# Performance work log

Hardware: AMD Instinct MI355X
Metric: run time of the kernel (lower is better)

The kernel has to match this reference:

```python
import jax, jax.numpy as jnp
import numpy as np
import math

B, S, D, H = 2, 2048, 512, 8
HD = D // H

def setup_inputs() -> dict:
    key = jax.random.key(0)
    ks = jax.random.split(key, 13)
    scale = 1.0 / math.sqrt(D)
    inp = {
        "q_in": jax.random.normal(ks[0], (B, S, D), jnp.float32),
        "k_in": jax.random.normal(ks[1], (B, S, D), jnp.float32),
        "v_in": jax.random.normal(ks[2], (B, S, D), jnp.float32),
        "mask": jax.random.randint(ks[3], (B, 1, S, S), 0, 2, jnp.int32),
        "W1": jax.random.uniform(ks[4], (D, D), jnp.float32, -scale, scale),
        "b1": jax.random.uniform(ks[5], (D,), jnp.float32, -scale, scale),
        "W2": jax.random.uniform(ks[6], (D, D), jnp.float32, -scale, scale),
        "b2": jax.random.uniform(ks[7], (D,), jnp.float32, -scale, scale),
        "W3": jax.random.uniform(ks[8], (D, D), jnp.float32, -scale, scale),
        "b3": jax.random.uniform(ks[9], (D,), jnp.float32, -scale, scale),
        "Wo": jax.random.uniform(ks[10], (D, D), jnp.float32, -scale, scale),
        "bo": jax.random.uniform(ks[11], (D,), jnp.float32, -scale, scale),
    }
    return inp

def reference(q_in, k_in, v_in, mask, W1, b1, W2, b2, W3, b3, Wo, bo):
    # Linear projections (torch Linear: y = x @ W.T + b)
    q = q_in @ W1.T + b1  # [B,S,D]
    k = k_in @ W2.T + b2
    v = v_in @ W3.T + b3
    # split heads -> [B,H,S,HD]
    def split(x):
        return x.reshape(B, S, H, HD).transpose(0, 2, 1, 3)
    q, k, v = split(q), split(k), split(v)
    scores = jnp.einsum("bhqd,bhkd->bhqk", q, k) / math.sqrt(HD)
    scores = jnp.where(mask == 0, jnp.float32(-1e9), scores)
    attn = jax.nn.softmax(scores, axis=-1)
    out = jnp.einsum("bhqk,bhkd->bhqd", attn, v)  # [B,H,S,HD]
    out = out.transpose(0, 2, 1, 3).reshape(B, S, D)
    return out @ Wo.T + bo
```

## Files before the change

kernel.cpp:

```cpp
#include <hip/hip_runtime.h>
#include <hip/hip_bf16.h>
#include <math.h>

constexpr int B_ = 2, S_ = 2048, D_ = 512, H_ = 8, HD_ = 64;
constexpr int M_ = B_ * S_;
constexpr int NT_ = S_ / 64;
constexpr int NSPLIT = 2;
constexpr int NT2 = NT_ / NSPLIT;
constexpr int ROWS = B_ * S_ * H_;

typedef short s16x8 __attribute__((ext_vector_type(8)));
typedef float f32x4 __attribute__((ext_vector_type(4)));
typedef unsigned short u16;
typedef unsigned long long u64;

#define SWZ(b) ((b) ^ ((((b) >> 7) & 7) << 4))

constexpr float SCL = 0.18033688f;
constexpr float FIXM = 12.0f;

static __device__ __forceinline__ unsigned int cvt_pk2(float lo, float hi) {
  __hip_bfloat162 h = __float22bfloat162_rn(make_float2(lo, hi));
  return *(unsigned int*)&h;
}
static __device__ __forceinline__ u16 cvt1(float f) {
  __hip_bfloat16 h = __float2bfloat16(f);
  return *(u16*)&h;
}
static __device__ __forceinline__ uint4 pack8(float4 a, float4 b) {
  uint4 r;
  r.x = cvt_pk2(a.x, a.y); r.y = cvt_pk2(a.z, a.w);
  r.z = cvt_pk2(b.x, b.y); r.w = cvt_pk2(b.z, b.w);
  return r;
}

#define QKV_STEP(BUF, T)                                                      \
  {                                                                           \
    const bool more_ = ((T) < 7);                                             \
    if (more_) {                                                              \
      const int o4 = ((T) + 1) * 16;                                          \
      fx[0] = Xb[o4]; fx[1] = Xb[o4 + 1]; fx[2] = Xb[o4 + 2]; fx[3] = Xb[o4 + 3]; \
      fw[0] = Wb[o4]; fw[1] = Wb[o4 + 1]; fw[2] = Wb[o4 + 2]; fw[3] = Wb[o4 + 3]; \
    }                                                                         \
    __builtin_amdgcn_s_setprio(1);                                            \
    _Pragma("unroll")                                                         \
    for (int kw = 0; kw < 2; ++kw) {                                          \
      s16x8 af0 = *(const s16x8*)(shb + SWZ((BUF)*16384 + (wm*32 + l15)*128 + kw*64 + lg*16)); \
      s16x8 af1 = *(const s16x8*)(shb + SWZ((BUF)*16384 + (wm*32 + 16 + l15)*128 + kw*64 + lg*16)); \
      s16x8 bf0 = *(const s16x8*)(shb + SWZ((BUF)*16384 + 8192 + (wn*32 + l15)*128 + kw*64 + lg*16)); \
      s16x8 bf1 = *(const s16x8*)(shb + SWZ((BUF)*16384 + 8192 + (wn*32 + 16 + l15)*128 + kw*64 + lg*16)); \
      acc[0][0] = __builtin_amdgcn_mfma_f32_16x16x32_bf16(af0, bf0, acc[0][0], 0, 0, 0); \
      acc[0][1] = __builtin_amdgcn_mfma_f32_16x16x32_bf16(af0, bf1, acc[0][1], 0, 0, 0); \
      acc[1][0] = __builtin_amdgcn_mfma_f32_16x16x32_bf16(af1, bf0, acc[1][0], 0, 0, 0); \
      acc[1][1] = __builtin_amdgcn_mfma_f32_16x16x32_bf16(af1, bf1, acc[1][1], 0, 0, 0); \
    }                                                                         \
    __builtin_amdgcn_s_setprio(0);                                            \
    if (more_) {                                                              \
      char* p_ = shb + ((BUF) ^ 1) * 16384;                                   \
      *(uint4*)(p_ + SWZ(awb)) = pack8(fx[0], fx[1]);                         \
      *(uint4*)(p_ + SWZ(awb + 16)) = pack8(fx[2], fx[3]);                    \
      *(uint4*)(p_ + SWZ(bwb)) = pack8(fw[0], fw[1]);                         \
      *(uint4*)(p_ + SWZ(bwb + 16)) = pack8(fw[2], fw[3]);                    \
    }                                                                         \
    __syncthreads();                                                          \
  }

__global__ __launch_bounds__(256) void gemm_qkv(
    const float* __restrict__ Xq, const float* __restrict__ Wq,
    const float* __restrict__ bq, u16* __restrict__ Yq,
    const float* __restrict__ Xk, const float* __restrict__ Wk,
    const float* __restrict__ bk, u16* __restrict__ Yk,
    const float* __restrict__ Xv, const float* __restrict__ Wv,
    const float* __restrict__ bv, u16* __restrict__ Yv,
    const int* __restrict__ mask, u64* __restrict__ mbits)
{
  const float* X; const float* W; const float* bias; u16* Y;
  const int z = blockIdx.z;
  if (z == 0)      { X = Xq; W = Wq; bias = bq; Y = Yq; }
  else if (z == 1) { X = Xk; W = Wk; bias = bk; Y = Yk; }
  else             { X = Xv; W = Wv; bias = bv; Y = Yv; }

  __shared__ __align__(128) u16 SH[2][2][64][64];
  char* shb = (char*)SH;

  const int tid = threadIdx.x;
  const int lane = tid & 63, w = tid >> 6;
  const int l15 = lane & 15, lg = lane >> 4;
  const int wm = w >> 1, wn = w & 1;
  const int m0 = blockIdx.x * 64, n0 = blockIdx.y * 64;
  const int sr = tid >> 2, sc = (tid & 3) * 16;

  const float4* Xb = (const float4*)&X[(size_t)(m0 + sr) * D_ + sc];
  const float4* Wb = (const float4*)&W[(size_t)(n0 + sr) * D_ + sc];
  const int awb = sr * 128 + (tid & 3) * 32;
  const int bwb = 8192 + sr * 128 + (tid & 3) * 32;

  f32x4 acc[2][2];
#pragma unroll
  for (int i = 0; i < 2; ++i)
#pragma unroll
    for (int j = 0; j < 2; ++j) acc[i][j] = (f32x4){0.f, 0.f, 0.f, 0.f};

  float4 fx[4], fw[4];
#pragma unroll
  for (int i = 0; i < 4; ++i) { fx[i] = Xb[i]; fw[i] = Wb[i]; }
  {
    char* p = shb;
    *(uint4*)(p + SWZ(awb)) = pack8(fx[0], fx[1]);
    *(uint4*)(p + SWZ(awb + 16)) = pack8(fx[2], fx[3]);
    *(uint4*)(p + SWZ(bwb)) = pack8(fw[0], fw[1]);
    *(uint4*)(p + SWZ(bwb + 16)) = pack8(fw[2], fw[3]);
  }
  __syncthreads();

#pragma unroll 1
  for (int tt = 0; tt < 8; tt += 2) {
    QKV_STEP(0, tt)
    QKV_STEP(1, tt + 1)
  }

  float bias_v[2];
  bias_v[0] = bias[n0 + wn * 32 + l15];
  bias_v[1] = bias[n0 + wn * 32 + 16 + l15];
  const float oscale = (z == 0) ? SCL : 1.0f;

  if (z != 2) {
#pragma unroll
    for (int am = 0; am < 2; ++am)
#pragma unroll
      for (int bn = 0; bn < 2; ++bn)
#pragma unroll
        for (int j = 0; j < 4; ++j) {
          const int row = m0 + wm * 32 + am * 16 + lg * 4 + j;
          const int col = n0 + wn * 32 + bn * 16 + l15;
          Y[(size_t)row * D_ + col] = cvt1((acc[am][bn][j] + bias_v[bn]) * oscale);
        }
  } else {
#pragma unroll
    for (int am = 0; am < 2; ++am)
#pragma unroll
      for (int bn = 0; bn < 2; ++bn) {
        const int dd = wn * 32 + bn * 16 + l15;
        const int sl = wm * 32 + am * 16 + lg * 4;
        ushort4 pk;
        pk.x = cvt1(acc[am][bn][0] + bias_v[bn]);
        pk.y = cvt1(acc[am][bn][1] + bias_v[bn]);
        pk.z = cvt1(acc[am][bn][2] + bias_v[bn]);
        pk.w = cvt1(acc[am][bn][3] + bias_v[bn]);
        *(ushort4*)(shb + SWZ(dd * 128 + sl * 2)) = pk;
      }
    __syncthreads();
    const int batch = m0 >> 11, sb = m0 & (S_ - 1);
    const int cr = sr * 128 + (tid & 3) * 32;
    uint4 c0 = *(uint4*)(shb + SWZ(cr));
    uint4 c1 = *(uint4*)(shb + SWZ(cr + 16));
    u16* dst = &Y[(((size_t)batch * H_ + blockIdx.y) * 64 + sr) * S_ + sb + sc];
    *(uint4*)dst = c0;
    *(uint4*)(dst + 8) = c1;
  }

  {
    const int bid = blockIdx.x + blockIdx.y * gridDim.x +
                    blockIdx.z * gridDim.x * gridDim.y;
    const int gw = bid * 4 + w;
    const int nslots = B_ * S_ * NT_;
#pragma unroll 1
    for (int s = gw * 4; s < nslots; s += 6144 * 4) {
      int v0 = mask[(size_t)(s + 0) * 64 + lane];
      int v1 = (s + 1 < nslots) ? mask[(size_t)(s + 1) * 64 + lane] : 0;
      int v2 = (s + 2 < nslots) ? mask[(size_t)(s + 2) * 64 + lane] : 0;
      int v3 = (s + 3 < nslots) ? mask[(size_t)(s + 3) * 64 + lane] : 0;
      u64 b0 = __ballot(v0 != 0);
      u64 b1 = __ballot(v1 != 0);
      u64 b2 = __ballot(v2 != 0);
      u64 b3 = __ballot(v3 != 0);
      if (lane == 0) {
        mbits[s] = b0;
        if (s + 1 < nslots) mbits[s + 1] = b1;
        if (s + 2 < nslots) mbits[s + 2] = b2;
        if (s + 3 < nslots) mbits[s + 3] = b3;
      }
    }
  }
}

#define OPROJ_STEP(BUF, T)                                                    \
  {                                                                           \
    const bool more_ = ((T) < 7);                                             \
    if (more_) {                                                              \
      const int k0 = ((T) + 1) * 64;                                          \
      ax[0] = ((const uint4*)(Xb + k0))[0];                                   \
      ax[1] = ((const uint4*)(Xb + k0))[1];                                   \
      const int o4 = ((T) + 1) * 16;                                          \
      fw[0] = Wb[o4]; fw[1] = Wb[o4 + 1]; fw[2] = Wb[o4 + 2]; fw[3] = Wb[o4 + 3]; \
    }                                                                         \
    __builtin_amdgcn_s_setprio(1);                                            \
    _Pragma("unroll")                                                         \
    for (int kw = 0; kw < 2; ++kw) {                                          \
      s16x8 af0 = *(const s16x8*)(shb + SWZ((BUF)*16384 + (wm*32 + l15)*128 + kw*64 + lg*16)); \
      s16x8 af1 = *(const s16x8*)(shb + SWZ((BUF)*16384 + (wm*32 + 16 + l15)*128 + kw*64 + lg*16)); \
      s16x8 bf0 = *(const s16x8*)(shb + SWZ((BUF)*16384 + 8192 + (wn*32 + l15)*128 + kw*64 + lg*16)); \
      s16x8 bf1 = *(const s16x8*)(shb + SWZ((BUF)*16384 + 8192 + (wn*32 + 16 + l15)*128 + kw*64 + lg*16)); \
      acc[0][0] = __builtin_amdgcn_mfma_f32_16x16x32_bf16(af0, bf0, acc[0][0], 0, 0, 0); \
      acc[0][1] = __builtin_amdgcn_mfma_f32_16x16x32_bf16(af0, bf1, acc[0][1], 0, 0, 0); \
      acc[1][0] = __builtin_amdgcn_mfma_f32_16x16x32_bf16(af1, bf0, acc[1][0], 0, 0, 0); \
      acc[1][1] = __builtin_amdgcn_mfma_f32_16x16x32_bf16(af1, bf1, acc[1][1], 0, 0, 0); \
    }                                                                         \
    __builtin_amdgcn_s_setprio(0);                                            \
    if (more_) {                                                              \
      char* p_ = shb + ((BUF) ^ 1) * 16384;                                   \
      *(uint4*)(p_ + SWZ(awb)) = ax[0];                                       \
      *(uint4*)(p_ + SWZ(awb + 16)) = ax[1];                                  \
      *(uint4*)(p_ + SWZ(bwb)) = pack8(fw[0], fw[1]);                         \
      *(uint4*)(p_ + SWZ(bwb + 16)) = pack8(fw[2], fw[3]);                    \
    }                                                                         \
    __syncthreads();                                                          \
  }

__global__ __launch_bounds__(256) void gemm_oproj(
    const u16* __restrict__ X, const float* __restrict__ W,
    const float* __restrict__ bias, float* __restrict__ Y)
{
  __shared__ __align__(128) u16 SH[2][2][64][64];
  char* shb = (char*)SH;

  const int tid = threadIdx.x;
  const int lane = tid & 63, w = tid >> 6;
  const int l15 = lane & 15, lg = lane >> 4;
  const int wm = w >> 1, wn = w & 1;
  const int m0 = blockIdx.x * 64, n0 = blockIdx.y * 64;
  const int sr = tid >> 2, sc = (tid & 3) * 16;

  const u16* Xb = X + (size_t)(m0 + sr) * D_ + sc;
  const float4* Wb = (const float4*)&W[(size_t)(n0 + sr) * D_ + sc];
  const int awb = sr * 128 + (tid & 3) * 32;
  const int bwb = 8192 + sr * 128 + (tid & 3) * 32;

  f32x4 acc[2][2];
#pragma unroll
  for (int i = 0; i < 2; ++i)
#pragma unroll
    for (int j = 0; j < 2; ++j) acc[i][j] = (f32x4){0.f, 0.f, 0.f, 0.f};

  uint4 ax[2]; float4 fw[4];
  ax[0] = ((const uint4*)Xb)[0]; ax[1] = ((const uint4*)Xb)[1];
#pragma unroll
  for (int i = 0; i < 4; ++i) fw[i] = Wb[i];
  {
    char* p = shb;
    *(uint4*)(p + SWZ(awb)) = ax[0];
    *(uint4*)(p + SWZ(awb + 16)) = ax[1];
    *(uint4*)(p + SWZ(bwb)) = pack8(fw[0], fw[1]);
    *(uint4*)(p + SWZ(bwb + 16)) = pack8(fw[2], fw[3]);
  }
  __syncthreads();

#pragma unroll 1
  for (int tt = 0; tt < 8; tt += 2) {
    OPROJ_STEP(0, tt)
    OPROJ_STEP(1, tt + 1)
  }

  float bias_v[2];
  bias_v[0] = bias[n0 + wn * 32 + l15];
  bias_v[1] = bias[n0 + wn * 32 + 16 + l15];
#pragma unroll
  for (int am = 0; am < 2; ++am)
#pragma unroll
    for (int bn = 0; bn < 2; ++bn)
#pragma unroll
      for (int j = 0; j < 4; ++j) {
        const int row = m0 + wm * 32 + am * 16 + lg * 4 + j;
        const int col = n0 + wn * 32 + bn * 16 + l15;
        Y[(size_t)row * D_ + col] = acc[am][bn][j] + bias_v[bn];
      }
}

__global__ __launch_bounds__(256) void attn_mfma(
    const u16* __restrict__ qp, const u16* __restrict__ kp,
    const u16* __restrict__ vt, const u64* __restrict__ mbits,
    float* __restrict__ po, float* __restrict__ pm, float* __restrict__ pl)
{
  const int b = blockIdx.z >> 1, half = blockIdx.z & 1;
  const int h = blockIdx.y;
  const int q0 = blockIdx.x * 64;
  const int kt0 = half * (S_ / NSPLIT);
  const int tid = threadIdx.x;
  const int lane = tid & 63;
  const int w = tid >> 6;
  const int l15 = lane & 15, lg = lane >> 4;

  __shared__ __align__(128) u16 KV[2][2][64][64];
  __shared__ __align__(128) u16 Pl[4][16][64];
  char* kvb = (char*)KV;
  char* plb = (char*)Pl;

  const int qr = q0 + w * 16;

  const u16* qrow = qp + ((size_t)b * S_ + qr + l15) * D_ + h * HD_;
  const s16x8 qf0 = *(const s16x8*)(qrow + lg * 8);
  const s16x8 qf1 = *(const s16x8*)(qrow + 32 + lg * 8);

  s16x8 onesf;
#pragma unroll
  for (int i = 0; i < 8; ++i) onesf[i] = (short)0x3F80;

  f32x4 out[4];
#pragma unroll
  for (int dt = 0; dt < 4; ++dt) out[dt] = (f32x4){0.f, 0.f, 0.f, 0.f};
  float l_s = 0.f;

  const int sr = tid >> 2;
  const int sc = (tid & 3) * 16;
  const u16* kbase = kp + (size_t)b * S_ * D_ + h * HD_;
  const u16* vbase = vt + (((size_t)b * H_ + h) * 64 + sr) * (size_t)S_ + kt0 + sc;
  const u64* mrow = mbits + ((size_t)b * S_ + qr + l15) * NT_ + half * NT2;

  const int pbase = w * 2048 + l15 * 128;

  uint4 rk0, rk1, rv0, rv1;
  {
    const u16* ksrc = kbase + (size_t)(kt0 + sr) * D_ + sc;
    rk0 = *(const uint4*)ksrc; rk1 = *(const uint4*)(ksrc + 8);
    rv0 = *(const uint4*)vbase; rv1 = *(const uint4*)(vbase + 8);
    const int kb = (sr << 7) + (tid & 3) * 32;
    const int vb = ((64 + sr) << 7) + (tid & 3) * 32;
    *(uint4*)(kvb + SWZ(kb)) = rk0; *(uint4*)(kvb + SWZ(kb + 16)) = rk1;
    *(uint4*)(kvb + SWZ(vb)) = rv0; *(uint4*)(kvb + SWZ(vb + 16)) = rv1;
  }
  u64 msk = mrow[0];
  __syncthreads();

#pragma unroll 1
  for (int t = 0; t < NT2; ++t) {
    const int cur = t & 1;
    const bool more = (t + 1 < NT2);
    u64 msk_n = 0;
    if (more) {
      const int kt = (t + 1) * 64;
      const u16* ksrc = kbase + (size_t)(kt0 + kt + sr) * D_ + sc;
      rk0 = *(const uint4*)ksrc; rk1 = *(const uint4*)(ksrc + 8);
      rv0 = *(const uint4*)(vbase + kt); rv1 = *(const uint4*)(vbase + kt + 8);
      msk_n = mrow[t + 1];
    }

    const u64 sh = msk >> (lg * 4);
    const int kbufbase = (cur * 2 + 0) * 64 * 128;
    const int vbufbase = (cur * 2 + 1) * 64 * 128;

    f32x4 z[4];
    __builtin_amdgcn_s_setprio(1);
#pragma unroll
    for (int t4 = 0; t4 < 4; ++t4) {
      const int kb = kbufbase + ((t4 * 16 + l15) << 7) + lg * 16;
      s16x8 kb0 = *(const s16x8*)(kvb + SWZ(kb));
      s16x8 kb1 = *(const s16x8*)(kvb + SWZ(kb + 64));
      f32x4 zz = (f32x4){0.f, 0.f, 0.f, 0.f};
      zz = __builtin_amdgcn_mfma_f32_16x16x32_bf16(kb0, qf0, zz, 0, 0, 0);
      zz = __builtin_amdgcn_mfma_f32_16x16x32_bf16(kb1, qf1, zz, 0, 0, 0);
      z[t4] = zz;
    }
    __builtin_amdgcn_s_setprio(0);

    float x[4][4];
#pragma unroll
    for (int t4 = 0; t4 < 4; ++t4) {
      unsigned int g = (unsigned int)(sh >> (t4 * 16)) & 0xFu;
#pragma unroll
      for (int r = 0; r < 4; ++r) {
        float xv = ((g >> r) & 1u) ? z[t4][r] : -1.0e9f;
        x[t4][r] = exp2f(xv - FIXM);
      }
    }

#pragma unroll
    for (int t4 = 0; t4 < 4; ++t4) {
      uint2 pk;
      pk.x = cvt_pk2(x[t4][0], x[t4][1]);
      pk.y = cvt_pk2(x[t4][2], x[t4][3]);
      *(uint2*)(plb + SWZ(pbase + t4 * 32 + lg * 8)) = pk;
    }

    s16x8 pa0 = *(const s16x8*)(plb + SWZ(pbase + lg * 16));
    s16x8 pa1 = *(const s16x8*)(plb + SWZ(pbase + 64 + lg * 16));

    __builtin_amdgcn_s_setprio(1);
    f32x4 zl = (f32x4){0.f, 0.f, 0.f, 0.f};
    zl = __builtin_amdgcn_mfma_f32_16x16x32_bf16(onesf, pa0, zl, 0, 0, 0);
    zl = __builtin_amdgcn_mfma_f32_16x16x32_bf16(onesf, pa1, zl, 0, 0, 0);
#pragma unroll
    for (int dt = 0; dt < 4; ++dt) {
      const int vb = vbufbase + ((dt * 16 + l15) << 7) + lg * 16;
      s16x8 va0 = *(const s16x8*)(kvb + SWZ(vb));
      s16x8 va1 = *(const s16x8*)(kvb + SWZ(vb + 64));
      out[dt] = __builtin_amdgcn_mfma_f32_16x16x32_bf16(va0, pa0, out[dt], 0, 0, 0);
      out[dt] = __builtin_amdgcn_mfma_f32_16x16x32_bf16(va1, pa1, out[dt], 0, 0, 0);
    }
    __builtin_amdgcn_s_setprio(0);
    l_s += zl[0];

    if (more) {
      const int nb = cur ^ 1;
      const int kb2 = (((nb * 2 + 0) * 64 + sr) << 7) + (tid & 3) * 32;
      const int vb2 = (((nb * 2 + 1) * 64 + sr) << 7) + (tid & 3) * 32;
      *(uint4*)(kvb + SWZ(kb2)) = rk0; *(uint4*)(kvb + SWZ(kb2 + 16)) = rk1;
      *(uint4*)(kvb + SWZ(vb2)) = rv0; *(uint4*)(kvb + SWZ(vb2 + 16)) = rv1;
      msk = msk_n;
    }
    __syncthreads();
  }

  const int rowi = ((b * S_ + qr + l15) * H_) + h;
  float* pobase = po + ((size_t)half * ROWS + rowi) * 64;
#pragma unroll
  for (int dt = 0; dt < 4; ++dt) {
    float4 o = make_float4(out[dt][0], out[dt][1], out[dt][2], out[dt][3]);
    *(float4*)&pobase[dt * 16 + lg * 4] = o;
  }
  if (lg == 0) {
    pm[(size_t)half * ROWS + rowi] = FIXM;
    pl[(size_t)half * ROWS + rowi] = l_s;
  }
}

__global__ __launch_bounds__(256) void attn_combine(
    const float* __restrict__ po, const float* __restrict__ pm,
    const float* __restrict__ pl, u16* __restrict__ ob)
{
  const int gid = blockIdx.x * 256 + threadIdx.x;
  const int row = gid >> 4;
  const int d0 = (gid & 15) * 4;

  float4 o1 = *(const float4*)&po[(size_t)row * 64 + d0];
  float4 o2 = *(const float4*)&po[(size_t)(ROWS + row) * 64 + d0];
  const float m1 = pm[row], m2 = pm[ROWS + row];
  const float l1 = pl[row], l2 = pl[ROWS + row];
  const float m = fmaxf(m1, m2);
  const float w1 = exp2f(m1 - m), w2 = exp2f(m2 - m);
  const float inv = 1.0f / (l1 * w1 + l2 * w2);

  const int bq = row >> 3, h = row & 7;
  uint2 o;
  o.x = cvt_pk2((o1.x * w1 + o2.x * w2) * inv, (o1.y * w1 + o2.y * w2) * inv);
  o.y = cvt_pk2((o1.z * w1 + o2.z * w2) * inv, (o1.w * w1 + o2.w * w2) * inv);
  *(uint2*)&ob[(size_t)bq * D_ + h * 64 + d0] = o;
}

extern "C" void kernel_launch(void* const* d_in, const int* in_sizes, int n_in,
                              void* d_out, int out_size, void* d_ws,
                              size_t ws_size, hipStream_t stream)
{
  const float* q_in = (const float*)d_in[0];
  const float* k_in = (const float*)d_in[1];
  const float* v_in = (const float*)d_in[2];
  const int*   mask = (const int*)d_in[3];
  const float* W1 = (const float*)d_in[4];
  const float* b1 = (const float*)d_in[5];
  const float* W2 = (const float*)d_in[6];
  const float* b2 = (const float*)d_in[7];
  const float* W3 = (const float*)d_in[8];
  const float* b3 = (const float*)d_in[9];
  const float* Wo = (const float*)d_in[10];
  const float* bo = (const float*)d_in[11];
  float* out = (float*)d_out;

  char* ws = (char*)d_ws;
  u16* qp = (u16*)ws;
  u16* kp = (u16*)(ws + (4u << 20));
  u16* vtp = (u16*)(ws + (8u << 20));
  u64* mbits = (u64*)(ws + (12u << 20));
  float* pm = (float*)(ws + (13u << 20));
  float* pl = (float*)(ws + (13u << 20) + (ROWS * NSPLIT * 4));
  float* po = (float*)(ws + (13u << 20) + (512u << 10));
  u16* ob = qp;

  dim3 blk(256);
  gemm_qkv<<<dim3(M_ / 64, D_ / 64, 3), blk, 0, stream>>>(
      q_in, W1, b1, qp, k_in, W2, b2, kp, v_in, W3, b3, vtp, mask, mbits);
  attn_mfma<<<dim3(S_ / 64, H_, B_ * NSPLIT), blk, 0, stream>>>(
      qp, kp, vtp, mbits, po, pm, pl);
  attn_combine<<<ROWS * 16 / 256, blk, 0, stream>>>(po, pm, pl, ob);
  gemm_oproj<<<dim3(M_ / 64, D_ / 64), blk, 0, stream>>>(ob, Wo, bo, out);
}
```

Before: 101.8 us.

## Widen QKV GEMM tile to 128 columns and vectorize mask bit packing

The QKV projection kernel now computes a 64x128 output tile per block, reusing each staged X tile across two weight halves. This halves the number of X reloads and fp32-to-bf16 conversions, at the cost of more registers and shared memory and half as many blocks. The mask-to-bitmask pass now reads int4 per lane and packs the ballots in a permuted bit order. The attention kernel's bit extraction is changed to match that order, so mask reads are wider and fewer.

```diff
diff --git a/kernel.cpp b/kernel.cpp
--- a/kernel.cpp
+++ b/kernel.cpp
@@ -39,28 +39,37 @@
     const bool more_ = ((T) < 7);                                             \
     if (more_) {                                                              \
       const int o4 = ((T) + 1) * 16;                                          \
-      fx[0] = Xb[o4]; fx[1] = Xb[o4 + 1]; fx[2] = Xb[o4 + 2]; fx[3] = Xb[o4 + 3]; \
-      fw[0] = Wb[o4]; fw[1] = Wb[o4 + 1]; fw[2] = Wb[o4 + 2]; fw[3] = Wb[o4 + 3]; \
+      fx[0] = Xb[o4];  fx[1] = Xb[o4 + 1];  fx[2] = Xb[o4 + 2];  fx[3] = Xb[o4 + 3]; \
+      fw0[0] = W0b[o4]; fw0[1] = W0b[o4 + 1]; fw0[2] = W0b[o4 + 2]; fw0[3] = W0b[o4 + 3]; \
+      fw1[0] = W1b[o4]; fw1[1] = W1b[o4 + 1]; fw1[2] = W1b[o4 + 2]; fw1[3] = W1b[o4 + 3]; \
     }                                                                         \
     __builtin_amdgcn_s_setprio(1);                                            \
     _Pragma("unroll")                                                         \
     for (int kw = 0; kw < 2; ++kw) {                                          \
-      s16x8 af0 = *(const s16x8*)(shb + SWZ((BUF)*16384 + (wm*32 + l15)*128 + kw*64 + lg*16)); \
-      s16x8 af1 = *(const s16x8*)(shb + SWZ((BUF)*16384 + (wm*32 + 16 + l15)*128 + kw*64 + lg*16)); \
-      s16x8 bf0 = *(const s16x8*)(shb + SWZ((BUF)*16384 + 8192 + (wn*32 + l15)*128 + kw*64 + lg*16)); \
-      s16x8 bf1 = *(const s16x8*)(shb + SWZ((BUF)*16384 + 8192 + (wn*32 + 16 + l15)*128 + kw*64 + lg*16)); \
-      acc[0][0] = __builtin_amdgcn_mfma_f32_16x16x32_bf16(af0, bf0, acc[0][0], 0, 0, 0); \
-      acc[0][1] = __builtin_amdgcn_mfma_f32_16x16x32_bf16(af0, bf1, acc[0][1], 0, 0, 0); \
-      acc[1][0] = __builtin_amdgcn_mfma_f32_16x16x32_bf16(af1, bf0, acc[1][0], 0, 0, 0); \
-      acc[1][1] = __builtin_amdgcn_mfma_f32_16x16x32_bf16(af1, bf1, acc[1][1], 0, 0, 0); \
+      s16x8 af0 = *(const s16x8*)(shb + SWZ((BUF)*24576 + (wm*32 + l15)*128 + kw*64 + lg*16)); \
+      s16x8 af1 = *(const s16x8*)(shb + SWZ((BUF)*24576 + (wm*32 + 16 + l15)*128 + kw*64 + lg*16)); \
+      s16x8 b00 = *(const s16x8*)(shb + SWZ((BUF)*24576 + 8192 + (wn*32 + l15)*128 + kw*64 + lg*16)); \
+      s16x8 b01 = *(const s16x8*)(shb + SWZ((BUF)*24576 + 8192 + (wn*32 + 16 + l15)*128 + kw*64 + lg*16)); \
+      s16x8 b10 = *(const s16x8*)(shb + SWZ((BUF)*24576 + 16384 + (wn*32 + l15)*128 + kw*64 + lg*16)); \
+      s16x8 b11 = *(const s16x8*)(shb + SWZ((BUF)*24576 + 16384 + (wn*32 + 16 + l15)*128 + kw*64 + lg*16)); \
+      acc[0][0][0] = __builtin_amdgcn_mfma_f32_16x16x32_bf16(af0, b00, acc[0][0][0], 0, 0, 0); \
+      acc[0][0][1] = __builtin_amdgcn_mfma_f32_16x16x32_bf16(af0, b01, acc[0][0][1], 0, 0, 0); \
+      acc[0][1][0] = __builtin_amdgcn_mfma_f32_16x16x32_bf16(af1, b00, acc[0][1][0], 0, 0, 0); \
+      acc[0][1][1] = __builtin_amdgcn_mfma_f32_16x16x32_bf16(af1, b01, acc[0][1][1], 0, 0, 0); \
+      acc[1][0][0] = __builtin_amdgcn_mfma_f32_16x16x32_bf16(af0, b10, acc[1][0][0], 0, 0, 0); \
+      acc[1][0][1] = __builtin_amdgcn_mfma_f32_16x16x32_bf16(af0, b11, acc[1][0][1], 0, 0, 0); \
+      acc[1][1][0] = __builtin_amdgcn_mfma_f32_16x16x32_bf16(af1, b10, acc[1][1][0], 0, 0, 0); \
+      acc[1][1][1] = __builtin_amdgcn_mfma_f32_16x16x32_bf16(af1, b11, acc[1][1][1], 0, 0, 0); \
     }                                                                         \
     __builtin_amdgcn_s_setprio(0);                                            \
     if (more_) {                                                              \
-      char* p_ = shb + ((BUF) ^ 1) * 16384;                                   \
+      char* p_ = shb + ((BUF) ^ 1) * 24576;                                   \
       *(uint4*)(p_ + SWZ(awb)) = pack8(fx[0], fx[1]);                         \
       *(uint4*)(p_ + SWZ(awb + 16)) = pack8(fx[2], fx[3]);                    \
-      *(uint4*)(p_ + SWZ(bwb)) = pack8(fw[0], fw[1]);                         \
-      *(uint4*)(p_ + SWZ(bwb + 16)) = pack8(fw[2], fw[3]);                    \
+      *(uint4*)(p_ + SWZ(b0wb)) = pack8(fw0[0], fw0[1]);                      \
+      *(uint4*)(p_ + SWZ(b0wb + 16)) = pack8(fw0[2], fw0[3]);                 \
+      *(uint4*)(p_ + SWZ(b1wb)) = pack8(fw1[0], fw1[1]);                      \
+      *(uint4*)(p_ + SWZ(b1wb + 16)) = pack8(fw1[2], fw1[3]);                 \
     }                                                                         \
     __syncthreads();                                                          \
   }
@@ -80,36 +89,42 @@
   else if (z == 1) { X = Xk; W = Wk; bias = bk; Y = Yk; }
   else             { X = Xv; W = Wv; bias = bv; Y = Yv; }
 
-  __shared__ __align__(128) u16 SH[2][2][64][64];
-  char* shb = (char*)SH;
+  __shared__ __align__(128) char SH[2][24576];
+  char* shb = &SH[0][0];
 
   const int tid = threadIdx.x;
   const int lane = tid & 63, w = tid >> 6;
   const int l15 = lane & 15, lg = lane >> 4;
   const int wm = w >> 1, wn = w & 1;
-  const int m0 = blockIdx.x * 64, n0 = blockIdx.y * 64;
+  const int m0 = blockIdx.x * 64, n0 = blockIdx.y * 128;
   const int sr = tid >> 2, sc = (tid & 3) * 16;
 
-  const float4* Xb = (const float4*)&X[(size_t)(m0 + sr) * D_ + sc];
-  const float4* Wb = (const float4*)&W[(size_t)(n0 + sr) * D_ + sc];
-  const int awb = sr * 128 + (tid & 3) * 32;
-  const int bwb = 8192 + sr * 128 + (tid & 3) * 32;
-
-  f32x4 acc[2][2];
-#pragma unroll
-  for (int i = 0; i < 2; ++i)
-#pragma unroll
-    for (int j = 0; j < 2; ++j) acc[i][j] = (f32x4){0.f, 0.f, 0.f, 0.f};
-
-  float4 fx[4], fw[4];
-#pragma unroll
-  for (int i = 0; i < 4; ++i) { fx[i] = Xb[i]; fw[i] = Wb[i]; }
+  const float4* Xb  = (const float4*)&X[(size_t)(m0 + sr) * D_ + sc];
+  const float4* W0b = (const float4*)&W[(size_t)(n0 + sr) * D_ + sc];
+  const float4* W1b = (const float4*)&W[(size_t)(n0 + 64 + sr) * D_ + sc];
+  const int awb  = sr * 128 + (tid & 3) * 32;
+  const int b0wb = 8192 + awb;
+  const int b1wb = 16384 + awb;
+
+  f32x4 acc[2][2][2];
+#pragma unroll
+  for (int nh = 0; nh < 2; ++nh)
+#pragma unroll
+    for (int i = 0; i < 2; ++i)
+#pragma unroll
+      for (int j = 0; j < 2; ++j) acc[nh][i][j] = (f32x4){0.f, 0.f, 0.f, 0.f};
+
+  float4 fx[4], fw0[4], fw1[4];
+#pragma unroll
+  for (int i = 0; i < 4; ++i) { fx[i] = Xb[i]; fw0[i] = W0b[i]; fw1[i] = W1b[i]; }
   {
     char* p = shb;
     *(uint4*)(p + SWZ(awb)) = pack8(fx[0], fx[1]);
     *(uint4*)(p + SWZ(awb + 16)) = pack8(fx[2], fx[3]);
-    *(uint4*)(p + SWZ(bwb)) = pack8(fw[0], fw[1]);
-    *(uint4*)(p + SWZ(bwb + 16)) = pack8(fw[2], fw[3]);
+    *(uint4*)(p + SWZ(b0wb)) = pack8(fw0[0], fw0[1]);
+    *(uint4*)(p + SWZ(b0wb + 16)) = pack8(fw0[2], fw0[3]);
+    *(uint4*)(p + SWZ(b1wb)) = pack8(fw1[0], fw1[1]);
+    *(uint4*)(p + SWZ(b1wb + 16)) = pack8(fw1[2], fw1[3]);
   }
   __syncthreads();
 
@@ -119,66 +134,76 @@
     QKV_STEP(1, tt + 1)
   }
 
-  float bias_v[2];
-  bias_v[0] = bias[n0 + wn * 32 + l15];
-  bias_v[1] = bias[n0 + wn * 32 + 16 + l15];
   const float oscale = (z == 0) ? SCL : 1.0f;
 
   if (z != 2) {
 #pragma unroll
-    for (int am = 0; am < 2; ++am)
-#pragma unroll
-      for (int bn = 0; bn < 2; ++bn)
-#pragma unroll
-        for (int j = 0; j < 4; ++j) {
-          const int row = m0 + wm * 32 + am * 16 + lg * 4 + j;
-          const int col = n0 + wn * 32 + bn * 16 + l15;
-          Y[(size_t)row * D_ + col] = cvt1((acc[am][bn][j] + bias_v[bn]) * oscale);
+    for (int nh = 0; nh < 2; ++nh) {
+      float bias_v[2];
+      bias_v[0] = bias[n0 + nh * 64 + wn * 32 + l15];
+      bias_v[1] = bias[n0 + nh * 64 + wn * 32 + 16 + l15];
+#pragma unroll
+      for (int am = 0; am < 2; ++am)
+#pragma unroll
+        for (int bn = 0; bn < 2; ++bn)
+#pragma unroll
+          for (int j = 0; j < 4; ++j) {
+            const int row = m0 + wm * 32 + am * 16 + lg * 4 + j;
+            const int col = n0 + nh * 64 + wn * 32 + bn * 16 + l15;
+            Y[(size_t)row * D_ + col] = cvt1((acc[nh][am][bn][j] + bias_v[bn]) * oscale);
+          }
+    }
+  } else {
+    const int batch = m0 >> 11, sb = m0 & (S_ - 1);
+#pragma unroll
+    for (int nh = 0; nh < 2; ++nh) {
+      const int hh = blockIdx.y * 2 + nh;
+      float bias_v[2];
+      bias_v[0] = bias[n0 + nh * 64 + wn * 32 + l15];
+      bias_v[1] = bias[n0 + nh * 64 + wn * 32 + 16 + l15];
+      __syncthreads();
+#pragma unroll
+      for (int am = 0; am < 2; ++am)
+#pragma unroll
+        for (int bn = 0; bn < 2; ++bn) {
+          const int dd = wn * 32 + bn * 16 + l15;
+          const int sl = wm * 32 + am * 16 + lg * 4;
+          ushort4 pk;
+          pk.x = cvt1(acc[nh][am][bn][0] + bias_v[bn]);
+          pk.y = cvt1(acc[nh][am][bn][1] + bias_v[bn]);
+          pk.z = cvt1(acc[nh][am][bn][2] + bias_v[bn]);
+          pk.w = cvt1(acc[nh][am][bn][3] + bias_v[bn]);
+          *(ushort4*)(shb + SWZ(dd * 128 + sl * 2)) = pk;
         }
-  } else {
-#pragma unroll
-    for (int am = 0; am < 2; ++am)
-#pragma unroll
-      for (int bn = 0; bn < 2; ++bn) {
-        const int dd = wn * 32 + bn * 16 + l15;
-        const int sl = wm * 32 + am * 16 + lg * 4;
-        ushort4 pk;
-        pk.x = cvt1(acc[am][bn][0] + bias_v[bn]);
-        pk.y = cvt1(acc[am][bn][1] + bias_v[bn]);
-        pk.z = cvt1(acc[am][bn][2] + bias_v[bn]);
-        pk.w = cvt1(acc[am][bn][3] + bias_v[bn]);
-        *(ushort4*)(shb + SWZ(dd * 128 + sl * 2)) = pk;
-      }
-    __syncthreads();
-    const int batch = m0 >> 11, sb = m0 & (S_ - 1);
-    const int cr = sr * 128 + (tid & 3) * 32;
-    uint4 c0 = *(uint4*)(shb + SWZ(cr));
-    uint4 c1 = *(uint4*)(shb + SWZ(cr + 16));
-    u16* dst = &Y[(((size_t)batch * H_ + blockIdx.y) * 64 + sr) * S_ + sb + sc];
-    *(uint4*)dst = c0;
-    *(uint4*)(dst + 8) = c1;
+      __syncthreads();
+      const int cr = sr * 128 + (tid & 3) * 32;
+      uint4 c0 = *(uint4*)(shb + SWZ(cr));
+      uint4 c1 = *(uint4*)(shb + SWZ(cr + 16));
+      u16* dst = &Y[(((size_t)batch * H_ + hh) * 64 + sr) * S_ + sb + sc];
+      *(uint4*)dst = c0;
+      *(uint4*)(dst + 8) = c1;
+    }
   }
 
   {
     const int bid = blockIdx.x + blockIdx.y * gridDim.x +
                     blockIdx.z * gridDim.x * gridDim.y;
     const int gw = bid * 4 + w;
-    const int nslots = B_ * S_ * NT_;
+    const int ngroups = (B_ * S_ * NT_) / 4;
 #pragma unroll 1
-    for (int s = gw * 4; s < nslots; s += 6144 * 4) {
-      int v0 = mask[(size_t)(s + 0) * 64 + lane];
-      int v1 = (s + 1 < nslots) ? mask[(size_t)(s + 1) * 64 + lane] : 0;
-      int v2 = (s + 2 < nslots) ? mask[(size_t)(s + 2) * 64 + lane] : 0;
-      int v3 = (s + 3 < nslots) ? mask[(size_t)(s + 3) * 64 + lane] : 0;
-      u64 b0 = __ballot(v0 != 0);
-      u64 b1 = __ballot(v1 != 0);
-      u64 b2 = __ballot(v2 != 0);
-      u64 b3 = __ballot(v3 != 0);
-      if (lane == 0) {
-        mbits[s] = b0;
-        if (s + 1 < nslots) mbits[s + 1] = b1;
-        if (s + 2 < nslots) mbits[s + 2] = b2;
-        if (s + 3 < nslots) mbits[s + 3] = b3;
+    for (int g = gw; g < ngroups; g += 3072) {
+      const int4 v = *(const int4*)&mask[(size_t)g * 256 + lane * 4];
+      u64 b0 = __ballot(v.x != 0);
+      u64 b1 = __ballot(v.y != 0);
+      u64 b2 = __ballot(v.z != 0);
+      u64 b3 = __ballot(v.w != 0);
+      if (lane < 4) {
+        const int q = lane;
+        u64 r = ((b0 >> (16 * q)) & 0xFFFFULL)
+              | (((b1 >> (16 * q)) & 0xFFFFULL) << 16)
+              | (((b2 >> (16 * q)) & 0xFFFFULL) << 32)
+              | (((b3 >> (16 * q)) & 0xFFFFULL) << 48);
+        mbits[(size_t)g * 4 + q] = r;
       }
     }
   }
@@ -344,7 +369,8 @@
       msk_n = mrow[t + 1];
     }
 
-    const u64 sh = msk >> (lg * 4);
+    const unsigned mlo = (unsigned)(msk >> lg);
+    const unsigned mhi = (unsigned)(msk >> (lg + 32));
     const int kbufbase = (cur * 2 + 0) * 64 * 128;
     const int vbufbase = (cur * 2 + 1) * 64 * 128;
 
@@ -365,10 +391,11 @@
     float x[4][4];
 #pragma unroll
     for (int t4 = 0; t4 < 4; ++t4) {
-      unsigned int g = (unsigned int)(sh >> (t4 * 16)) & 0xFu;
 #pragma unroll
       for (int r = 0; r < 4; ++r) {
-        float xv = ((g >> r) & 1u) ? z[t4][r] : -1.0e9f;
+        const unsigned bit = (r < 2) ? ((mlo >> (16 * r + 4 * t4)) & 1u)
+                                     : ((mhi >> (16 * (r - 2) + 4 * t4)) & 1u);
+        float xv = bit ? z[t4][r] : -1.0e9f;
         x[t4][r] = exp2f(xv - FIXM);
       }
     }
@@ -475,7 +502,7 @@
   u16* ob = qp;
 
   dim3 blk(256);
-  gemm_qkv<<<dim3(M_ / 64, D_ / 64, 3), blk, 0, stream>>>(
+  gemm_qkv<<<dim3(M_ / 64, D_ / 128, 3), blk, 0, stream>>>(
       q_in, W1, b1, qp, k_in, W2, b2, kp, v_in, W3, b3, vtp, mask, mbits);
   attn_mfma<<<dim3(S_ / 64, H_, B_ * NSPLIT), blk, 0, stream>>>(
       qp, kp, vtp, mbits, po, pm, pl);
```

Result: faster. 97.32 us (-4.4%).
